# Kernel tuning notes

Measured on AMD Instinct MI355X. Metric: run time of the kernel, lower is better.

Reference implementation:

```python
import jax, jax.numpy as jnp
import numpy as np

D_IN = 1024
D_OUT = 1024
NUM_HEADS = 16
HEAD_DIM = D_OUT // NUM_HEADS


def setup_inputs() -> dict:
    key = jax.random.key(0)
    ks = jax.random.split(key, 9)
    s = 0.02
    return {
        "x": jax.random.normal(ks[0], (2, 2048, D_IN), dtype=jnp.float32),
        "Wq": jax.random.normal(ks[1], (D_IN, D_OUT), dtype=jnp.float32) * s,
        "bq": jnp.zeros((D_OUT,), dtype=jnp.float32),
        "Wk": jax.random.normal(ks[2], (D_IN, D_OUT), dtype=jnp.float32) * s,
        "bk": jnp.zeros((D_OUT,), dtype=jnp.float32),
        "Wv": jax.random.normal(ks[3], (D_IN, D_OUT), dtype=jnp.float32) * s,
        "bv": jnp.zeros((D_OUT,), dtype=jnp.float32),
        "Wo": jax.random.normal(ks[4], (D_OUT, D_OUT), dtype=jnp.float32) * s,
        "bo": jnp.zeros((D_OUT,), dtype=jnp.float32),
    }


def reference(x, Wq, bq, Wk, bk, Wv, bv, Wo, bo):
    B, S, _ = x.shape
    H, Dh = NUM_HEADS, HEAD_DIM
    q = (x @ Wq + bq).reshape(B, S, H, Dh).transpose(0, 2, 1, 3)  # bhsd
    k = (x @ Wk + bk).reshape(B, S, H, Dh).transpose(0, 2, 1, 3)
    v = (x @ Wv + bv).reshape(B, S, H, Dh).transpose(0, 2, 1, 3)
    scores = jnp.einsum("bhqd,bhkd->bhqk", q, k) * (Dh ** -0.5)
    causal = jnp.tril(jnp.ones((S, S), dtype=bool))
    scores = jnp.where(causal, scores, jnp.float32(-jnp.inf))
    w = jax.nn.softmax(scores, axis=-1)
    ctx = jnp.einsum("bhqk,bhkd->bhqd", w, v)
    ctx = ctx.transpose(0, 2, 1, 3).reshape(B, S, H * Dh)
    return ctx @ Wo + bo
```

## Files before the change

### kernel.cpp

```cpp
#include <hip/hip_runtime.h>
#include <cmath>

#define D_IN 1024
#define D_OUT 1024
#define NUM_HEADS 16
#define HEAD_DIM 64
#define BATCH 2
#define SEQ 2048
#define GK 1024
#define KT 32

typedef __attribute__((ext_vector_type(8))) short short8;
typedef __attribute__((ext_vector_type(4))) short short4v;
typedef __attribute__((ext_vector_type(4))) float float4v;
typedef __attribute__((ext_vector_type(16))) float f32x16;
typedef __attribute__((ext_vector_type(2))) int int2v;

__device__ __forceinline__ unsigned short f2bf(float f) {
  unsigned int u = __builtin_bit_cast(unsigned int, f);
  unsigned int r = (u + 0x7FFFu + ((u >> 16) & 1u)) >> 16;
  return (unsigned short)r;
}
__device__ __forceinline__ float bf2f(unsigned short h) {
  return __builtin_bit_cast(float, (unsigned int)h << 16);
}

__device__ __forceinline__ unsigned int cvtpk(float lo, float hi) {
  unsigned int r;
  asm("v_cvt_pk_bf16_f32 %0, %1, %2" : "=v"(r) : "v"(lo), "v"(hi));
  return r;
}

__device__ __forceinline__ void async_copy16(void* lds, const void* g) {
  __builtin_amdgcn_global_load_lds(
      (const __attribute__((address_space(1))) unsigned int*)g,
      (__attribute__((address_space(3))) unsigned int*)lds, 16, 0, 0);
}

__global__ __launch_bounds__(256) void prep(
    const float* __restrict__ x, const float* __restrict__ Wq,
    const float* __restrict__ Wk, const float* __restrict__ Wv,
    const float* __restrict__ Wo, unsigned short* __restrict__ xb,
    unsigned short* __restrict__ wqkv_t, unsigned short* __restrict__ wo_t) {
  const int z = blockIdx.z;
  if (z == 4) {
    const int bid = blockIdx.y * 32 + blockIdx.x;
    const size_t i0 = ((size_t)bid * 256 + threadIdx.x) * 16;
#pragma unroll
    for (int half = 0; half < 2; ++half) {
      const size_t o = i0 + half * 8;
      float4 a = *(const float4*)(x + o);
      float4 b = *(const float4*)(x + o + 4);
      union { unsigned short u[8]; short8 v; } t;
      t.u[0] = f2bf(a.x); t.u[1] = f2bf(a.y); t.u[2] = f2bf(a.z); t.u[3] = f2bf(a.w);
      t.u[4] = f2bf(b.x); t.u[5] = f2bf(b.y); t.u[6] = f2bf(b.z); t.u[7] = f2bf(b.w);
      *(short8*)(xb + o) = t.v;
    }
    return;
  }
  const float* W = (z == 0) ? Wq : (z == 1) ? Wk : (z == 2) ? Wv : Wo;
  unsigned short* out = (z < 3) ? (wqkv_t + (size_t)z * 1024 * 1024) : wo_t;

  __shared__ float T[32][33];
  const int r = threadIdx.x >> 3;
  const int c4 = (threadIdx.x & 7) << 2;
  const int k0 = blockIdx.x * 32, n0 = blockIdx.y * 32;

  float4 v = *(const float4*)(W + (size_t)(k0 + r) * 1024 + n0 + c4);
  T[r][c4 + 0] = v.x; T[r][c4 + 1] = v.y; T[r][c4 + 2] = v.z; T[r][c4 + 3] = v.w;
  __syncthreads();

  union { unsigned short u[4]; short4v v4; } o;
#pragma unroll
  for (int i = 0; i < 4; ++i) o.u[i] = f2bf(T[c4 + i][r]);
  *(short4v*)(out + (size_t)(n0 + r) * 1024 + k0 + c4) = o.v4;
}

__device__ __forceinline__ void gemm_core(
    const unsigned short* __restrict__ A, const unsigned short* __restrict__ Bt,
    unsigned short* As, unsigned short* Bs, int bm, int bn, float4v acc[4][4]) {
  const int tid = threadIdx.x;
  const int wave = tid >> 6, lane = tid & 63;
  const int quad = lane >> 4, l16 = lane & 15;
  const int wr = wave >> 1, wc = wave & 1;
  const int sw = l16 & 7;

  int srow[4], sgc[4];
#pragma unroll
  for (int t = 0; t < 4; ++t) {
    const int c = (wave * 4 + t) * 64 + lane;
    srow[t] = c >> 3;
    sgc[t] = ((c & 7) ^ (srow[t] & 7)) * 8;
  }

  for (int k0 = 0; k0 < GK; k0 += 64) {
    __syncthreads();
#pragma unroll
    for (int t = 0; t < 4; ++t) {
      const int c = (wave * 4 + t) * 64 + lane;
      async_copy16(As + (size_t)c * 8, A + (size_t)(bm + srow[t]) * GK + k0 + sgc[t]);
    }
#pragma unroll
    for (int t = 0; t < 4; ++t) {
      const int c = (wave * 4 + t) * 64 + lane;
      async_copy16(Bs + (size_t)c * 8, Bt + (size_t)(bn + srow[t]) * GK + k0 + sgc[t]);
    }
    __syncthreads();

#pragma unroll
    for (int h = 0; h < 2; ++h) {
      short8 af[4], bfr[4];
#pragma unroll
      for (int i = 0; i < 4; ++i) {
        const int row = wr * 64 + i * 16 + l16;
        af[i] = *(const short8*)&As[((size_t)row * 8 + ((h * 4 + quad) ^ sw)) * 8];
      }
#pragma unroll
      for (int j = 0; j < 4; ++j) {
        const int row = wc * 64 + j * 16 + l16;
        bfr[j] = *(const short8*)&Bs[((size_t)row * 8 + ((h * 4 + quad) ^ sw)) * 8];
      }
#pragma unroll
      for (int i = 0; i < 4; ++i)
#pragma unroll
        for (int j = 0; j < 4; ++j)
          acc[i][j] = __builtin_amdgcn_mfma_f32_16x16x32_bf16(af[i], bfr[j], acc[i][j], 0, 0, 0);
    }
  }
}

__global__ __launch_bounds__(256) void gemm_qkv(
    const unsigned short* __restrict__ A, const unsigned short* __restrict__ Bt,
    const float* __restrict__ bq, const float* __restrict__ bk,
    const float* __restrict__ bv,
    unsigned short* __restrict__ qbuf, unsigned short* __restrict__ kblk,
    unsigned short* __restrict__ vblk) {
  __shared__ unsigned short SMEM[128 * 136];
  const int tid = threadIdx.x;
  const int wave = tid >> 6, lane = tid & 63;
  const int quad = lane >> 4, l16 = lane & 15;
  const int wr = wave >> 1, wc = wave & 1;
  const int bm = blockIdx.x * 128, bn = blockIdx.y * 128;

  float4v acc[4][4] = {};
  gemm_core(A, Bt, SMEM, SMEM + 8192, bm, bn, acc);

  __syncthreads();

  const int seg = bn >> 10;
  const int nb0 = bn & 1023;
  const float* bias = (seg == 0) ? bq : (seg == 1) ? bk : bv;
  const float scale = (seg == 0) ? 0.18033688011112043f : 1.0f;

#pragma unroll
  for (int j = 0; j < 4; ++j) {
    const int nl = wc * 64 + j * 16 + l16;
    const float bsv = bias[nb0 + nl];
#pragma unroll
    for (int i = 0; i < 4; ++i) {
#pragma unroll
      for (int r = 0; r < 4; ++r) {
        const int ml = wr * 64 + i * 16 + quad * 4 + r;
        SMEM[ml * 136 + nl] = f2bf((acc[i][j][r] + bsv) * scale);
      }
    }
  }
  __syncthreads();

  const int b = bm >> 11;
  const int s0 = bm & 2047;

  if (seg == 0) {
#pragma unroll
    for (int it = 0; it < 8; ++it) {
      const int linear = it * 256 + tid;
      const int d3 = linear & 7;
      const int sl = (linear >> 3) & 127;
      const int h = linear >> 10;
      const short8 vv = *(const short8*)&SMEM[sl * 136 + h * 64 + d3 * 8];
      const int bh = b * NUM_HEADS + (nb0 >> 6) + h;
      *(short8*)&qbuf[((size_t)bh * SEQ + s0 + sl) * HEAD_DIM + d3 * 8] = vv;
    }
  } else if (seg == 1) {
#pragma unroll
    for (int it = 0; it < 8; ++it) {
      const int linear = it * 256 + tid;
      const int key = linear & 31;
      const int hb = (linear >> 5) & 1;
      const int f = (linear >> 6) & 3;
      const int st = (linear >> 8) & 3;
      const int h = linear >> 10;
      const int ml = st * 32 + key;
      const int nl = h * 64 + f * 16 + hb * 8;
      const short8 vv = *(const short8*)&SMEM[ml * 136 + nl];
      const int bh = b * NUM_HEADS + (nb0 >> 6) + h;
      const int stg = (s0 >> 5) + st;
      *(short8*)&kblk[((size_t)bh * 64 + stg) * 2048 + f * 512 + hb * 256 + key * 8] = vv;
    }
  } else {
#pragma unroll
    for (int it = 0; it < 8; ++it) {
      const int linear = it * 256 + tid;
      const int d31 = linear & 31;
      const int s8 = (linear >> 5) & 1;
      const int dt = (linear >> 6) & 1;
      const int kk = (linear >> 7) & 1;
      const int st = (linear >> 8) & 3;
      const int h = linear >> 10;
      const int nl = h * 64 + dt * 32 + d31;
      const int mlb = st * 32 + kk * 16 + s8 * 8;
      union { unsigned short u[8]; short8 v; } vv;
#pragma unroll
      for (int s0i = 0; s0i < 8; ++s0i)
        vv.u[s0i] = SMEM[(mlb + s0i) * 136 + nl];
      const int bh = b * NUM_HEADS + (nb0 >> 6) + h;
      const int stg = (s0 >> 5) + st;
      *(short8*)&vblk[((size_t)bh * 64 + stg) * 2048 + (kk * 2 + dt) * 512 +
                      s8 * 256 + d31 * 8] = vv.v;
    }
  }
}

__global__ __launch_bounds__(256) void gemm_out(
    const unsigned short* __restrict__ A, const unsigned short* __restrict__ Bt,
    const float* __restrict__ bo, float* __restrict__ out) {
  __shared__ unsigned short As[128 * 64];
  __shared__ unsigned short Bs[128 * 64];
  const int wave = threadIdx.x >> 6, lane = threadIdx.x & 63;
  const int quad = lane >> 4, l16 = lane & 15;
  const int wr = wave >> 1, wc = wave & 1;
  const int bm = blockIdx.x * 128, bn = blockIdx.y * 128;

  float4v acc[4][4] = {};
  gemm_core(A, Bt, As, Bs, bm, bn, acc);

#pragma unroll
  for (int j = 0; j < 4; ++j) {
    const int n = bn + wc * 64 + j * 16 + l16;
    const float bsv = bo[n];
#pragma unroll
    for (int i = 0; i < 4; ++i) {
#pragma unroll
      for (int r = 0; r < 4; ++r) {
        const int m = bm + wr * 64 + i * 16 + quad * 4 + r;
        out[(size_t)m * D_OUT + n] = acc[i][j][r] + bsv;
      }
    }
  }
}

#define OBS 72

__global__ __launch_bounds__(256) void attn_kernel(
    const unsigned short* __restrict__ qf, const unsigned short* __restrict__ kblk,
    const unsigned short* __restrict__ vblk, unsigned short* __restrict__ ctx) {
  __shared__ unsigned short OB[4 * 32 * OBS];
  __shared__ float LL[4 * 32];

  const int id = blockIdx.x;
  const int bh = id & 31;
  const int qblk = 63 - (id >> 5);
  const int qw0 = qblk * 32;
  const int tid = threadIdx.x;
  const int w = tid >> 6;
  const int lane = tid & 63;
  const int l32 = lane & 31;
  const int hi = lane >> 5;

  const int nt = qblk + 1;
  const int qch = (nt + 3) >> 2;
  const int t0 = w * qch;
  const int t1 = min(nt, t0 + qch);

  const size_t bh_base = (size_t)bh * SEQ * HEAD_DIM;
  const unsigned short* kb = kblk + bh_base + (size_t)lane * 8;
  const unsigned short* vb = vblk + bh_base + (size_t)lane * 8;

  short8 qfr[4];
  {
    const unsigned short* qrow =
        qf + bh_base + (size_t)(qw0 + l32) * HEAD_DIM + hi * 8;
#pragma unroll
    for (int f = 0; f < 4; ++f) qfr[f] = *(const short8*)(qrow + f * 16);
  }

  f32x16 O0 = {}, O1 = {};
  float l_part = 0.f;

  if (t0 < t1) {
    short8 kA[4], vA[4], kB[4], vB[4];

    auto load = [&](int kt, short8 kd[4], short8 vd[4]) {
      const size_t base = (size_t)kt * 2048;
#pragma unroll
      for (int f = 0; f < 4; ++f) kd[f] = *(const short8*)(kb + base + f * 512);
#pragma unroll
      for (int f = 0; f < 4; ++f) vd[f] = *(const short8*)(vb + base + f * 512);
    };

    auto step = [&](int kt, const short8 kd[4], const short8 vd[4], bool masked) {
      (void)kt;
      f32x16 s = {};
#pragma unroll
      for (int f = 0; f < 4; ++f)
        s = __builtin_amdgcn_mfma_f32_32x32x16_bf16(kd[f], qfr[f], s, 0, 0, 0);

      float p[16];
#pragma unroll
      for (int g = 0; g < 4; ++g)
#pragma unroll
        for (int r = 0; r < 4; ++r) {
          float sv = s[g * 4 + r];
          if (masked) {
            const int krow = r + 8 * g + 4 * hi;
            sv = (krow <= l32) ? sv : -1e30f;
          }
          const float pv = __builtin_exp2f(sv);
          p[g * 4 + r] = pv;
          l_part += pv;
        }

      unsigned int c[8];
#pragma unroll
      for (int g = 0; g < 4; ++g) {
        c[g * 2 + 0] = cvtpk(p[g * 4 + 0], p[g * 4 + 1]);
        c[g * 2 + 1] = cvtpk(p[g * 4 + 2], p[g * 4 + 3]);
      }
      {
        int2v r0 = __builtin_amdgcn_permlane32_swap((int)c[0], (int)c[2], false, false);
        c[0] = (unsigned int)r0.x; c[2] = (unsigned int)r0.y;
        int2v r1 = __builtin_amdgcn_permlane32_swap((int)c[1], (int)c[3], false, false);
        c[1] = (unsigned int)r1.x; c[3] = (unsigned int)r1.y;
        int2v r2 = __builtin_amdgcn_permlane32_swap((int)c[4], (int)c[6], false, false);
        c[4] = (unsigned int)r2.x; c[6] = (unsigned int)r2.y;
        int2v r3 = __builtin_amdgcn_permlane32_swap((int)c[5], (int)c[7], false, false);
        c[5] = (unsigned int)r3.x; c[7] = (unsigned int)r3.y;
      }
      union { unsigned int d[4]; short8 v; } pa0, pa1;
      pa0.d[0] = c[0]; pa0.d[1] = c[1]; pa0.d[2] = c[2]; pa0.d[3] = c[3];
      pa1.d[0] = c[4]; pa1.d[1] = c[5]; pa1.d[2] = c[6]; pa1.d[3] = c[7];

      O0 = __builtin_amdgcn_mfma_f32_32x32x16_bf16(pa0.v, vd[0], O0, 0, 0, 0);
      O1 = __builtin_amdgcn_mfma_f32_32x32x16_bf16(pa0.v, vd[1], O1, 0, 0, 0);
      O0 = __builtin_amdgcn_mfma_f32_32x32x16_bf16(pa1.v, vd[2], O0, 0, 0, 0);
      O1 = __builtin_amdgcn_mfma_f32_32x32x16_bf16(pa1.v, vd[3], O1, 0, 0, 0);
    };

    load(t0, kA, vA);
    int kt = t0;
    while (true) {
      const bool lastA = (kt == t1 - 1);
      if (!lastA) load(kt + 1, kB, vB);
      step(kt, kA, vA, kt == nt - 1);
      if (lastA) break;
      ++kt;
      const bool lastB = (kt == t1 - 1);
      if (!lastB) load(kt + 1, kA, vA);
      step(kt, kB, vB, kt == nt - 1);
      if (lastB) break;
      ++kt;
    }
  }

  const float lsum = l_part + __shfl_xor(l_part, 32);
  if (hi == 0) LL[w * 32 + l32] = lsum;
#pragma unroll
  for (int g = 0; g < 4; ++g)
#pragma unroll
    for (int r = 0; r < 4; ++r) {
      const int reg = g * 4 + r;
      const int row = r + 8 * g + 4 * hi;
      OB[(w * 32 + row) * OBS + l32] = f2bf(O0[reg]);
      OB[(w * 32 + row) * OBS + 32 + l32] = f2bf(O1[reg]);
    }

  __syncthreads();

  const int row = w * 8 + (lane >> 3);
  const int col0 = (lane & 7) * 8;
  float acc[8] = {};
#pragma unroll
  for (int u = 0; u < 4; ++u) {
    const short8 t = *(const short8*)&OB[(u * 32 + row) * OBS + col0];
#pragma unroll
    for (int i = 0; i < 8; ++i) acc[i] += bf2f((unsigned short)t[i]);
  }
  const float inv = 1.0f / (LL[row] + LL[32 + row] + LL[64 + row] + LL[96 + row]);
  union { unsigned short u[8]; short8 v; } o;
#pragma unroll
  for (int i = 0; i < 8; ++i) o.u[i] = f2bf(acc[i] * inv);
  const int b = bh >> 4, h = bh & 15;
  const int qg = qw0 + row;
  *(short8*)(ctx + ((size_t)b * SEQ + qg) * D_OUT + h * HEAD_DIM + col0) = o.v;
}

extern "C" void kernel_launch(void* const* d_in, const int* in_sizes, int n_in,
                              void* d_out, int out_size, void* d_ws, size_t ws_size,
                              hipStream_t stream) {
  const float* x  = (const float*)d_in[0];
  const float* Wq = (const float*)d_in[1];
  const float* bq = (const float*)d_in[2];
  const float* Wk = (const float*)d_in[3];
  const float* bk = (const float*)d_in[4];
  const float* Wv = (const float*)d_in[5];
  const float* bv = (const float*)d_in[6];
  const float* Wo = (const float*)d_in[7];
  const float* bo = (const float*)d_in[8];
  float* out = (float*)d_out;

  const int M = BATCH * SEQ;
  unsigned short* xb     = (unsigned short*)d_ws;
  unsigned short* wqkv_t = xb + (size_t)M * D_IN;
  unsigned short* wo_t   = wqkv_t + (size_t)3 * D_OUT * D_IN;
  unsigned short* qb     = wo_t + (size_t)D_OUT * D_OUT;
  unsigned short* kblk   = qb + (size_t)M * D_OUT;
  unsigned short* vblk   = kblk + (size_t)M * D_OUT;
  unsigned short* cb     = vblk + (size_t)M * D_OUT;

  prep<<<dim3(32, 32, 5), 256, 0, stream>>>(x, Wq, Wk, Wv, Wo, xb, wqkv_t, wo_t);
  gemm_qkv<<<dim3(M / 128, 3 * D_OUT / 128), 256, 0, stream>>>(
      xb, wqkv_t, bq, bk, bv, qb, kblk, vblk);
  attn_kernel<<<dim3(32 * 64), 256, 0, stream>>>(qb, kblk, vblk, cb);
  gemm_out<<<dim3(M / 128, D_OUT / 128), 256, 0, stream>>>(cb, wo_t, bo, out);
}
```

Before: 191.8 us.

## Double-buffer GEMM LDS tiles, remap blocks for XCD locality, use packed bf16 convert

Shared GEMM core now double-buffers the A/B LDS tiles, issuing async copies for the next k-tile before computing the current one and waiting with vmcnt so loads overlap MFMA work. Both GEMM kernels remap block IDs so consecutive blocks on the same XCD share tiles, aiming at better L2 reuse. The x-to-bf16 conversion in prep switches to a packed convert instruction. The cost is double the LDS footprint, which may lower occupancy.

```diff
diff --git a/kernel.cpp b/kernel.cpp
--- a/kernel.cpp
+++ b/kernel.cpp
@@ -9,6 +9,7 @@
 #define SEQ 2048
 #define GK 1024
 #define KT 32
+#define NT_K (GK / 64)
 
 typedef __attribute__((ext_vector_type(8))) short short8;
 typedef __attribute__((ext_vector_type(4))) short short4v;
@@ -51,9 +52,9 @@
       const size_t o = i0 + half * 8;
       float4 a = *(const float4*)(x + o);
       float4 b = *(const float4*)(x + o + 4);
-      union { unsigned short u[8]; short8 v; } t;
-      t.u[0] = f2bf(a.x); t.u[1] = f2bf(a.y); t.u[2] = f2bf(a.z); t.u[3] = f2bf(a.w);
-      t.u[4] = f2bf(b.x); t.u[5] = f2bf(b.y); t.u[6] = f2bf(b.z); t.u[7] = f2bf(b.w);
+      union { unsigned int d[4]; short8 v; } t;
+      t.d[0] = cvtpk(a.x, a.y); t.d[1] = cvtpk(a.z, a.w);
+      t.d[2] = cvtpk(b.x, b.y); t.d[3] = cvtpk(b.z, b.w);
       *(short8*)(xb + o) = t.v;
     }
     return;
@@ -76,49 +77,63 @@
   *(short4v*)(out + (size_t)(n0 + r) * 1024 + k0 + c4) = o.v4;
 }
 
+__device__ __forceinline__ void stage_tile(
+    const unsigned short* __restrict__ A, const unsigned short* __restrict__ Bt,
+    unsigned short* S, int buf, int bm, int bn, int k0, int wave, int lane) {
+  unsigned short* As = S + buf * 16384;
+  unsigned short* Bs = As + 8192;
+#pragma unroll
+  for (int t = 0; t < 4; ++t) {
+    const int c = (wave * 4 + t) * 64 + lane;
+    const int srow = c >> 3;
+    const int sgc = ((c & 7) ^ (srow & 7)) * 8;
+    async_copy16(As + (size_t)c * 8, A + (size_t)(bm + srow) * GK + k0 + sgc);
+  }
+#pragma unroll
+  for (int t = 0; t < 4; ++t) {
+    const int c = (wave * 4 + t) * 64 + lane;
+    const int srow = c >> 3;
+    const int sgc = ((c & 7) ^ (srow & 7)) * 8;
+    async_copy16(Bs + (size_t)c * 8, Bt + (size_t)(bn + srow) * GK + k0 + sgc);
+  }
+}
+
 __device__ __forceinline__ void gemm_core(
     const unsigned short* __restrict__ A, const unsigned short* __restrict__ Bt,
-    unsigned short* As, unsigned short* Bs, int bm, int bn, float4v acc[4][4]) {
+    unsigned short* S, int bm, int bn, float4v acc[4][4]) {
   const int tid = threadIdx.x;
   const int wave = tid >> 6, lane = tid & 63;
   const int quad = lane >> 4, l16 = lane & 15;
   const int wr = wave >> 1, wc = wave & 1;
   const int sw = l16 & 7;
 
-  int srow[4], sgc[4];
-#pragma unroll
-  for (int t = 0; t < 4; ++t) {
-    const int c = (wave * 4 + t) * 64 + lane;
-    srow[t] = c >> 3;
-    sgc[t] = ((c & 7) ^ (srow[t] & 7)) * 8;
-  }
-
-  for (int k0 = 0; k0 < GK; k0 += 64) {
-    __syncthreads();
-#pragma unroll
-    for (int t = 0; t < 4; ++t) {
-      const int c = (wave * 4 + t) * 64 + lane;
-      async_copy16(As + (size_t)c * 8, A + (size_t)(bm + srow[t]) * GK + k0 + sgc[t]);
-    }
-#pragma unroll
-    for (int t = 0; t < 4; ++t) {
-      const int c = (wave * 4 + t) * 64 + lane;
-      async_copy16(Bs + (size_t)c * 8, Bt + (size_t)(bn + srow[t]) * GK + k0 + sgc[t]);
-    }
-    __syncthreads();
-
+  stage_tile(A, Bt, S, 0, bm, bn, 0, wave, lane);
+
+  for (int t = 0; t < NT_K; ++t) {
+    if (t + 1 < NT_K) {
+      stage_tile(A, Bt, S, (t + 1) & 1, bm, bn, (t + 1) * 64, wave, lane);
+      asm volatile("s_waitcnt vmcnt(8)" ::: "memory");
+    } else {
+      asm volatile("s_waitcnt vmcnt(0)" ::: "memory");
+    }
+    __builtin_amdgcn_sched_barrier(0);
+    __builtin_amdgcn_s_barrier();
+    __builtin_amdgcn_sched_barrier(0);
+
+    const unsigned short* Asc = S + (t & 1) * 16384;
+    const unsigned short* Bsc = Asc + 8192;
 #pragma unroll
     for (int h = 0; h < 2; ++h) {
       short8 af[4], bfr[4];
 #pragma unroll
       for (int i = 0; i < 4; ++i) {
         const int row = wr * 64 + i * 16 + l16;
-        af[i] = *(const short8*)&As[((size_t)row * 8 + ((h * 4 + quad) ^ sw)) * 8];
+        af[i] = *(const short8*)&Asc[((size_t)row * 8 + ((h * 4 + quad) ^ sw)) * 8];
       }
 #pragma unroll
       for (int j = 0; j < 4; ++j) {
         const int row = wc * 64 + j * 16 + l16;
-        bfr[j] = *(const short8*)&Bs[((size_t)row * 8 + ((h * 4 + quad) ^ sw)) * 8];
+        bfr[j] = *(const short8*)&Bsc[((size_t)row * 8 + ((h * 4 + quad) ^ sw)) * 8];
       }
 #pragma unroll
       for (int i = 0; i < 4; ++i)
@@ -126,6 +141,10 @@
         for (int j = 0; j < 4; ++j)
           acc[i][j] = __builtin_amdgcn_mfma_f32_16x16x32_bf16(af[i], bfr[j], acc[i][j], 0, 0, 0);
     }
+
+    __builtin_amdgcn_sched_barrier(0);
+    __builtin_amdgcn_s_barrier();
+    __builtin_amdgcn_sched_barrier(0);
   }
 }
 
@@ -135,15 +154,18 @@
     const float* __restrict__ bv,
     unsigned short* __restrict__ qbuf, unsigned short* __restrict__ kblk,
     unsigned short* __restrict__ vblk) {
-  __shared__ unsigned short SMEM[128 * 136];
+  __shared__ unsigned short SMEM[2 * 128 * 64 * 2];
   const int tid = threadIdx.x;
   const int wave = tid >> 6, lane = tid & 63;
   const int quad = lane >> 4, l16 = lane & 15;
   const int wr = wave >> 1, wc = wave & 1;
-  const int bm = blockIdx.x * 128, bn = blockIdx.y * 128;
+
+  const int lid = blockIdx.y * 32 + blockIdx.x;
+  const int nid = (lid & 7) * 96 + (lid >> 3);
+  const int bm = (nid & 31) * 128, bn = (nid >> 5) * 128;
 
   float4v acc[4][4] = {};
-  gemm_core(A, Bt, SMEM, SMEM + 8192, bm, bn, acc);
+  gemm_core(A, Bt, SMEM, bm, bn, acc);
 
   __syncthreads();
 
@@ -224,15 +246,17 @@
 __global__ __launch_bounds__(256) void gemm_out(
     const unsigned short* __restrict__ A, const unsigned short* __restrict__ Bt,
     const float* __restrict__ bo, float* __restrict__ out) {
-  __shared__ unsigned short As[128 * 64];
-  __shared__ unsigned short Bs[128 * 64];
+  __shared__ unsigned short S[2 * 128 * 64 * 2];
   const int wave = threadIdx.x >> 6, lane = threadIdx.x & 63;
   const int quad = lane >> 4, l16 = lane & 15;
   const int wr = wave >> 1, wc = wave & 1;
-  const int bm = blockIdx.x * 128, bn = blockIdx.y * 128;
+
+  const int lid = blockIdx.y * 32 + blockIdx.x;
+  const int nid = (lid & 7) * 32 + (lid >> 3);
+  const int bm = (nid & 31) * 128, bn = (nid >> 5) * 128;
 
   float4v acc[4][4] = {};
-  gemm_core(A, Bt, As, Bs, bm, bn, acc);
+  gemm_core(A, Bt, S, bm, bn, acc);
 
 #pragma unroll
   for (int j = 0; j < 4; ++j) {
```

After: 178.5 us. -7.0%, faster.
